# Kernel tuning notes

Hardware: AMD Instinct MI355X
Metric: run time of the kernel (lower is better)

The kernel has to match this reference:

```python
import jax, jax.numpy as jnp
import numpy as np

H = 256
OUT = 2
FANOUT = 10
RES_N = [200000, 50000, 12000, 4096]
USER_N = [250000, 60000, 20000, 8192]
B = RES_N[-1]


def setup_inputs() -> dict:
    key = jax.random.key(0)
    ks = jax.random.split(key, 40)
    ki = iter(ks)
    rng = np.random.default_rng(0)
    inp = {}
    inp["res_x"] = jax.random.normal(next(ki), (RES_N[0], H), jnp.float32)
    inp["user_x"] = jax.random.normal(next(ki), (USER_N[0], H), jnp.float32)
    for name, N in (("res", RES_N), ("user", USER_N)):
        for i in range(3):
            n_src, n_dst = N[i], N[i + 1]
            E = n_dst * FANOUT
            row = jax.random.randint(next(ki), (E,), 0, n_src)   # source node ids
            col = jnp.repeat(jnp.arange(n_dst), FANOUT)          # target node ids
            inp[f"{name}_ei{i}"] = jnp.stack([row, col]).astype(jnp.int32)
    counts = rng.integers(10, 31, size=B)                        # ragged users per restaurant
    T = int(counts.sum())
    inp["num_users_per_res"] = jnp.asarray(counts, jnp.int32)
    inp["inverse_idx"] = jax.random.randint(next(ki), (T,), 0, USER_N[-1])

    def lin(k, fi, fo):
        return jax.random.normal(k, (fo, fi), jnp.float32) / np.sqrt(fi)

    for name in ("res", "user"):
        for i in range(3):
            inp[f"{name}_Wl{i}"] = lin(next(ki), H, H)
            inp[f"{name}_bl{i}"] = jnp.zeros((H,), jnp.float32)
            inp[f"{name}_Wr{i}"] = lin(next(ki), H, H)
    inp["W_out"] = lin(next(ki), 2 * H, OUT)
    inp["b_out"] = jnp.zeros((OUT,), jnp.float32)
    return inp


def sage_conv(x_src, x_tgt, edge_index, Wl, bl, Wr):
    """PyG SAGEConv (aggr='mean', bipartite): lin_l(mean_j x_j) + lin_r(x_tgt)."""
    n_tgt = x_tgt.shape[0]
    msgs = x_src[edge_index[0]]                                            # [E, H] gather
    s = jax.ops.segment_sum(msgs, edge_index[1], num_segments=n_tgt)      # [n_tgt, H]
    cnt = jax.ops.segment_sum(jnp.ones((edge_index.shape[1],), x_src.dtype),
                              edge_index[1], num_segments=n_tgt)
    agg = s / jnp.maximum(cnt, 1.0)[:, None]
    return agg @ Wl.T + bl + x_tgt @ Wr.T


def gnn_forward(x, eis, params, N):
    # ReLU (and dropout, identity in eval) applied when i != num_layers-1 == 1
    for i, (ei, (Wl, bl, Wr)) in enumerate(zip(eis, params)):
        x_tgt = x[: N[i + 1]]
        x = sage_conv(x, x_tgt, ei, Wl, bl, Wr)
        if i != 1:
            x = jax.nn.relu(x)
    return x


def reference(res_x, user_x,
              res_ei0, res_ei1, res_ei2,
              user_ei0, user_ei1, user_ei2,
              inverse_idx, num_users_per_res,
              res_Wl0, res_bl0, res_Wr0,
              res_Wl1, res_bl1, res_Wr1,
              res_Wl2, res_bl2, res_Wr2,
              user_Wl0, user_bl0, user_Wr0,
              user_Wl1, user_bl1, user_Wr1,
              user_Wl2, user_bl2, user_Wr2,
              W_out, b_out):
    res_params = [(res_Wl0, res_bl0, res_Wr0), (res_Wl1, res_bl1, res_Wr1), (res_Wl2, res_bl2, res_Wr2)]
    user_params = [(user_Wl0, user_bl0, user_Wr0), (user_Wl1, user_bl1, user_Wr1), (user_Wl2, user_bl2, user_Wr2)]
    res_out = gnn_forward(res_x, (res_ei0, res_ei1, res_ei2), res_params, RES_N)      # [B, H]
    user_out = gnn_forward(user_x, (user_ei0, user_ei1, user_ei2), user_params, USER_N)  # [M, H]
    # ragged segment-mean pooling: split by num_users_per_res, mean each group
    u = user_out[inverse_idx]                                              # [T, H]
    T = inverse_idx.shape[0]
    seg_ids = jnp.repeat(jnp.arange(B), num_users_per_res, total_repeat_length=T)
    pooled = jax.ops.segment_sum(u, seg_ids, num_segments=B)
    pooled = pooled / num_users_per_res.astype(pooled.dtype)[:, None]      # [B, H]
    emb = jnp.concatenate([res_out, pooled], axis=1)                       # [B, 2H]
    return emb @ W_out.T + b_out
```

## Files before the change

kernel.cpp:

```cpp
#include <hip/hip_runtime.h>

#define H 256
#define FANOUT 10

typedef __attribute__((ext_vector_type(8))) short bf16x8;
typedef __attribute__((ext_vector_type(4))) float f32x4;

__device__ __forceinline__ unsigned short f2bf(float x) {
  unsigned int u = __float_as_uint(x);
  u += 0x7FFFu + ((u >> 16) & 1u);
  return (unsigned short)(u >> 16);
}
__device__ __forceinline__ float bf2f(unsigned short h) {
  return __uint_as_float(((unsigned int)h) << 16);
}

struct PtrPack { const float* p[12]; };

__global__ __launch_bounds__(256) void wprep_kernel(PtrPack pk,
                                                    unsigned short* __restrict__ WB) {
  int g = blockIdx.x * 256 + threadIdx.x;
  int mat = g >> 16;
  int e = g & 65535;
  float x = pk.p[mat][e];
  unsigned short h = f2bf(x);
  float r = x - bf2f(h);
  WB[(size_t)mat * 131072 + e] = h;
  WB[(size_t)mat * 131072 + 65536 + e] = f2bf(r);
}

__global__ __launch_bounds__(256) void agg_kernel(
    const float* __restrict__ src, const int* __restrict__ row,
    float* __restrict__ agg, int n_tgt) {
  const int t = blockIdx.x * 4 + (threadIdx.x >> 6);
  if (t >= n_tgt) return;
  const int lane = threadIdx.x & 63;
  const int base = t * FANOUT;
  float4 acc = {0.f, 0.f, 0.f, 0.f};
#pragma unroll
  for (int k = 0; k < FANOUT; ++k) {
    int r = row[base + k];
    const float4 v =
        *reinterpret_cast<const float4*>(src + (size_t)r * H + lane * 4);
    acc.x += v.x; acc.y += v.y; acc.z += v.z; acc.w += v.w;
  }
  acc.x *= 0.1f; acc.y *= 0.1f; acc.z *= 0.1f; acc.w *= 0.1f;
  *reinterpret_cast<float4*>(agg + (size_t)t * H + lane * 4) = acc;
}

__global__ __launch_bounds__(256, 2) void sage_gemm_mfma(
    const float* __restrict__ Af, const float* __restrict__ Xf,
    const unsigned short* __restrict__ Wl2, const unsigned short* __restrict__ Wr2,
    const float* __restrict__ bias, float* __restrict__ Out,
    int n_tgt, int relu) {
  __shared__ unsigned short lds[2][2][4 * 64 * 8];
  const int tid = threadIdx.x;
  const int lane = tid & 63, wc = tid >> 6;
  const int l15 = lane & 15, lk = lane >> 4;
  const int m0 = blockIdx.x * 64;
  const int srow = tid >> 2, sch = tid & 3;
  const int grow = m0 + srow;
  const bool sok = grow < n_tgt;
  const int ldsoff = (((srow >> 4) * 64) + (srow & 15) + sch * 16) * 8;

  f32x4 acc[4][4];
#pragma unroll
  for (int i = 0; i < 4; ++i)
#pragma unroll
    for (int j = 0; j < 4; ++j) acc[i][j] = (f32x4){0.f, 0.f, 0.f, 0.f};

  float4 f0 = {0, 0, 0, 0}, f1 = {0, 0, 0, 0};
  auto gload = [&](int s) {
    if (sok) {
      const float* S = (s >> 3) ? Xf : Af;
      const float* p = S + (size_t)grow * H + (s & 7) * 32 + sch * 8;
      f0 = *reinterpret_cast<const float4*>(p);
      f1 = *reinterpret_cast<const float4*>(p + 4);
    } else {
      f0 = (float4){0, 0, 0, 0};
      f1 = (float4){0, 0, 0, 0};
    }
  };
  auto sconv = [&](int buf) {
    const float xs[8] = {f0.x, f0.y, f0.z, f0.w, f1.x, f1.y, f1.z, f1.w};
    bf16x8 vh, vl;
#pragma unroll
    for (int i = 0; i < 8; ++i) {
      unsigned short h = f2bf(xs[i]);
      vh[i] = (short)h;
      vl[i] = (short)f2bf(xs[i] - bf2f(h));
    }
    *reinterpret_cast<bf16x8*>(&lds[buf][0][ldsoff]) = vh;
    *reinterpret_cast<bf16x8*>(&lds[buf][1][ldsoff]) = vl;
  };

  gload(0);
  sconv(0);
  __syncthreads();

  for (int s = 0; s < 16; ++s) {
    const int buf = s & 1;
    if (s < 15) gload(s + 1);
    const int kt = (s & 7) * 32;
    const unsigned short* __restrict__ W = (s >> 3) ? Wr2 : Wl2;
    bf16x8 bh[4], bl[4];
#pragma unroll
    for (int nf = 0; nf < 4; ++nf) {
      const int off = (wc * 64 + nf * 16 + l15) * H + kt + lk * 8;
      bh[nf] = *reinterpret_cast<const bf16x8*>(W + off);
      bl[nf] = *reinterpret_cast<const bf16x8*>(W + 65536 + off);
    }
    bf16x8 ah[4], al[4];
#pragma unroll
    for (int mf = 0; mf < 4; ++mf) {
      const int o = (mf * 64 + lane) * 8;
      ah[mf] = *reinterpret_cast<const bf16x8*>(&lds[buf][0][o]);
      al[mf] = *reinterpret_cast<const bf16x8*>(&lds[buf][1][o]);
    }
#pragma unroll
    for (int mf = 0; mf < 4; ++mf)
#pragma unroll
      for (int nf = 0; nf < 4; ++nf) {
        acc[mf][nf] = __builtin_amdgcn_mfma_f32_16x16x32_bf16(ah[mf], bh[nf], acc[mf][nf], 0, 0, 0);
        acc[mf][nf] = __builtin_amdgcn_mfma_f32_16x16x32_bf16(ah[mf], bl[nf], acc[mf][nf], 0, 0, 0);
        acc[mf][nf] = __builtin_amdgcn_mfma_f32_16x16x32_bf16(al[mf], bh[nf], acc[mf][nf], 0, 0, 0);
      }
    if (s < 15) sconv(buf ^ 1);
    __syncthreads();
  }

#pragma unroll
  for (int nf = 0; nf < 4; ++nf) {
    const int c = wc * 64 + nf * 16 + l15;
    const float bv = bias[c];
#pragma unroll
    for (int mf = 0; mf < 4; ++mf) {
      const int r0 = m0 + mf * 16 + lk * 4;
#pragma unroll
      for (int j = 0; j < 4; ++j) {
        const int r = r0 + j;
        if (r < n_tgt) {
          float v = acc[mf][nf][j] + bv;
          if (relu) v = fmaxf(v, 0.f);
          Out[(size_t)r * H + c] = v;
        }
      }
    }
  }
}

__global__ __launch_bounds__(1024) void scan_kernel(
    const int* __restrict__ cnt, int* __restrict__ off, int B) {
  __shared__ int sdata[1024];
  const int t = threadIdx.x;
  const int base = t * 4;
  int c[4];
#pragma unroll
  for (int k = 0; k < 4; ++k) c[k] = (base + k < B) ? cnt[base + k] : 0;
  int s0 = c[0];
  int s1 = s0 + c[1];
  int s2 = s1 + c[2];
  int s3 = s2 + c[3];
  sdata[t] = s3;
  __syncthreads();
  for (int o = 1; o < 1024; o <<= 1) {
    int v = (t >= o) ? sdata[t - o] : 0;
    __syncthreads();
    sdata[t] += v;
    __syncthreads();
  }
  int excl = sdata[t] - s3;
  if (base + 0 < B) off[base + 0] = excl;
  if (base + 1 < B) off[base + 1] = excl + s0;
  if (base + 2 < B) off[base + 2] = excl + s1;
  if (base + 3 < B) off[base + 3] = excl + s2;
  if (t == 1023) off[B] = sdata[1023];
}

__global__ __launch_bounds__(256) void pool_kernel(
    const float* __restrict__ uo, const int* __restrict__ idx,
    const int* __restrict__ off, const int* __restrict__ cnt,
    float* __restrict__ pooled) {
  const int b = blockIdx.x * 4 + (threadIdx.x >> 6);
  const int lane = threadIdx.x & 63;
  const int o = off[b];
  const int n = cnt[b];
  float4 acc = {0.f, 0.f, 0.f, 0.f};
  for (int k = 0; k < n; ++k) {
    int u = idx[o + k];
    const float4 v =
        *reinterpret_cast<const float4*>(uo + (size_t)u * H + lane * 4);
    acc.x += v.x; acc.y += v.y; acc.z += v.z; acc.w += v.w;
  }
  const float inv = 1.0f / (float)n;
  acc.x *= inv; acc.y *= inv; acc.z *= inv; acc.w *= inv;
  *reinterpret_cast<float4*>(pooled + (size_t)b * H + lane * 4) = acc;
}

__global__ __launch_bounds__(256) void out_kernel(
    const float* __restrict__ res_out, const float* __restrict__ pooled,
    const float* __restrict__ Wout, const float* __restrict__ bout,
    float* __restrict__ out) {
  const int b = blockIdx.x;
  const int t = threadIdx.x;
  const float e0 = res_out[(size_t)b * H + t];
  const float e1 = pooled[(size_t)b * H + t];
  float p0 = e0 * Wout[t] + e1 * Wout[256 + t];
  float p1 = e0 * Wout[512 + t] + e1 * Wout[768 + t];
#pragma unroll
  for (int o = 32; o >= 1; o >>= 1) {
    p0 += __shfl_down(p0, o, 64);
    p1 += __shfl_down(p1, o, 64);
  }
  __shared__ float s0[4], s1[4];
  const int w = t >> 6, lane = t & 63;
  if (lane == 0) { s0[w] = p0; s1[w] = p1; }
  __syncthreads();
  if (t == 0) out[(size_t)b * 2 + 0] = s0[0] + s0[1] + s0[2] + s0[3] + bout[0];
  if (t == 1) out[(size_t)b * 2 + 1] = s1[0] + s1[1] + s1[2] + s1[3] + bout[1];
}

extern "C" void kernel_launch(void* const* d_in, const int* in_sizes, int n_in,
                              void* d_out, int out_size, void* d_ws,
                              size_t ws_size, hipStream_t stream) {
  const float* res_x  = (const float*)d_in[0];
  const float* user_x = (const float*)d_in[1];
  const int* res_ei[3]  = {(const int*)d_in[2], (const int*)d_in[3], (const int*)d_in[4]};
  const int* user_ei[3] = {(const int*)d_in[5], (const int*)d_in[6], (const int*)d_in[7]};

  const int* counts;
  const int* inv_idx;
  if (in_sizes[8] == 4096) { counts = (const int*)d_in[8]; inv_idx = (const int*)d_in[9]; }
  else                     { counts = (const int*)d_in[9]; inv_idx = (const int*)d_in[8]; }

  const float* rW[9]; const float* uW[9];
  for (int i = 0; i < 9; ++i) rW[i] = (const float*)d_in[10 + i];
  for (int i = 0; i < 9; ++i) uW[i] = (const float*)d_in[19 + i];
  const float* Wout = (const float*)d_in[28];
  const float* bout = (const float*)d_in[29];

  float* ws = (float*)d_ws;
  float* AGG  = ws;
  float* B1   = AGG  + (size_t)60000 * H;
  float* B2   = B1   + (size_t)60000 * H;
  float* U3   = B2   + (size_t)20000 * H;
  float* R3   = U3   + (size_t)8192  * H;
  float* POOL = R3   + (size_t)4096  * H;
  unsigned short* WB = (unsigned short*)(POOL + (size_t)4096 * H);
  int* OFF = (int*)(WB + (size_t)12 * 131072);

  PtrPack pk;
  pk.p[0] = uW[0]; pk.p[1] = uW[2];
  pk.p[2] = uW[3]; pk.p[3] = uW[5];
  pk.p[4] = uW[6]; pk.p[5] = uW[8];
  pk.p[6] = rW[0]; pk.p[7] = rW[2];
  pk.p[8] = rW[3]; pk.p[9] = rW[5];
  pk.p[10] = rW[6]; pk.p[11] = rW[8];
  wprep_kernel<<<3072, 256, 0, stream>>>(pk, WB);

  auto Wm = [&](int m) { return WB + (size_t)m * 131072; };
  auto gemm_grid = [](int n) { return (n + 63) / 64; };
  auto agg_grid = [](int n) { return (n + 3) / 4; };

  agg_kernel<<<agg_grid(60000), 256, 0, stream>>>(user_x, user_ei[0], AGG, 60000);
  sage_gemm_mfma<<<gemm_grid(60000), 256, 0, stream>>>(
      AGG, user_x, Wm(0), Wm(1), uW[1], B1, 60000, 1);
  agg_kernel<<<agg_grid(20000), 256, 0, stream>>>(B1, user_ei[1], AGG, 20000);
  sage_gemm_mfma<<<gemm_grid(20000), 256, 0, stream>>>(
      AGG, B1, Wm(2), Wm(3), uW[4], B2, 20000, 0);
  agg_kernel<<<agg_grid(8192), 256, 0, stream>>>(B2, user_ei[2], AGG, 8192);
  sage_gemm_mfma<<<gemm_grid(8192), 256, 0, stream>>>(
      AGG, B2, Wm(4), Wm(5), uW[7], U3, 8192, 1);

  agg_kernel<<<agg_grid(50000), 256, 0, stream>>>(res_x, res_ei[0], AGG, 50000);
  sage_gemm_mfma<<<gemm_grid(50000), 256, 0, stream>>>(
      AGG, res_x, Wm(6), Wm(7), rW[1], B1, 50000, 1);
  agg_kernel<<<agg_grid(12000), 256, 0, stream>>>(B1, res_ei[1], AGG, 12000);
  sage_gemm_mfma<<<gemm_grid(12000), 256, 0, stream>>>(
      AGG, B1, Wm(8), Wm(9), rW[4], B2, 12000, 0);
  agg_kernel<<<agg_grid(4096), 256, 0, stream>>>(B2, res_ei[2], AGG, 4096);
  sage_gemm_mfma<<<gemm_grid(4096), 256, 0, stream>>>(
      AGG, B2, Wm(10), Wm(11), rW[7], R3, 4096, 1);

  scan_kernel<<<1, 1024, 0, stream>>>(counts, OFF, 4096);
  pool_kernel<<<1024, 256, 0, stream>>>(U3, inv_idx, OFF, counts, POOL);
  out_kernel<<<4096, 256, 0, stream>>>(R3, POOL, Wout, bout, (float*)d_out);
}
```

Baseline: 1.068 ms.

## Batch user and restaurant GNN layers into joint launches, prefetch weights, fuse pool+out

Each SAGE layer's aggregation and GEMM for the user and restaurant towers now run in a single launch, with the tower chosen per block. This halves the number of launches and fills the GPU better on the small later layers. The GEMM main loop is unrolled by two and double-buffers the bf16 weight fragments in registers, so global weight loads overlap the MFMAs. Pooling and the output projection are fused into one kernel where four waves split each segment, removing the pooled intermediate buffer. The cost is a larger workspace, since per-tower buffers are no longer reused, and higher register pressure in the GEMM.

```diff
diff --git a/kernel.cpp b/kernel.cpp
--- a/kernel.cpp
+++ b/kernel.cpp
@@ -29,11 +29,23 @@
   WB[(size_t)mat * 131072 + 65536 + e] = f2bf(r);
 }
 
-__global__ __launch_bounds__(256) void agg_kernel(
-    const float* __restrict__ src, const int* __restrict__ row,
-    float* __restrict__ agg, int n_tgt) {
-  const int t = blockIdx.x * 4 + (threadIdx.x >> 6);
-  if (t >= n_tgt) return;
+__global__ __launch_bounds__(256) void agg_pair(
+    const float* __restrict__ srcU, const int* __restrict__ rowU,
+    float* __restrict__ aggU, int nU4,
+    const float* __restrict__ srcR, const int* __restrict__ rowR,
+    float* __restrict__ aggR) {
+  const int blk = blockIdx.x;
+  const float* __restrict__ src;
+  const int* __restrict__ row;
+  float* __restrict__ agg;
+  int t;
+  if (blk < nU4) {
+    src = srcU; row = rowU; agg = aggU;
+    t = blk * 4 + (threadIdx.x >> 6);
+  } else {
+    src = srcR; row = rowR; agg = aggR;
+    t = (blk - nU4) * 4 + (threadIdx.x >> 6);
+  }
   const int lane = threadIdx.x & 63;
   const int base = t * FANOUT;
   float4 acc = {0.f, 0.f, 0.f, 0.f};
@@ -49,15 +61,28 @@
 }
 
 __global__ __launch_bounds__(256, 2) void sage_gemm_mfma(
-    const float* __restrict__ Af, const float* __restrict__ Xf,
-    const unsigned short* __restrict__ Wl2, const unsigned short* __restrict__ Wr2,
-    const float* __restrict__ bias, float* __restrict__ Out,
-    int n_tgt, int relu) {
+    const float* __restrict__ AfU, const float* __restrict__ XfU,
+    const unsigned short* __restrict__ WlU, const unsigned short* __restrict__ WrU,
+    const float* __restrict__ bU, float* __restrict__ OutU, int nU,
+    const float* __restrict__ AfR, const float* __restrict__ XfR,
+    const unsigned short* __restrict__ WlR, const unsigned short* __restrict__ WrR,
+    const float* __restrict__ bR, float* __restrict__ OutR, int nR,
+    int relu) {
   __shared__ unsigned short lds[2][2][4 * 64 * 8];
+  const int nbU = (nU + 63) >> 6;
+  const bool isU = (int)blockIdx.x < nbU;
+  const float* __restrict__ Af = isU ? AfU : AfR;
+  const float* __restrict__ Xf = isU ? XfU : XfR;
+  const unsigned short* __restrict__ Wl2 = isU ? WlU : WlR;
+  const unsigned short* __restrict__ Wr2 = isU ? WrU : WrR;
+  const float* __restrict__ bias = isU ? bU : bR;
+  float* __restrict__ Out = isU ? OutU : OutR;
+  const int n_tgt = isU ? nU : nR;
+  const int m0 = (isU ? (int)blockIdx.x : (int)blockIdx.x - nbU) * 64;
+
   const int tid = threadIdx.x;
   const int lane = tid & 63, wc = tid >> 6;
   const int l15 = lane & 15, lk = lane >> 4;
-  const int m0 = blockIdx.x * 64;
   const int srow = tid >> 2, sch = tid & 3;
   const int grow = m0 + srow;
   const bool sok = grow < n_tgt;
@@ -93,30 +118,25 @@
     *reinterpret_cast<bf16x8*>(&lds[buf][0][ldsoff]) = vh;
     *reinterpret_cast<bf16x8*>(&lds[buf][1][ldsoff]) = vl;
   };
-
-  gload(0);
-  sconv(0);
-  __syncthreads();
-
-  for (int s = 0; s < 16; ++s) {
-    const int buf = s & 1;
-    if (s < 15) gload(s + 1);
+  auto loadB = [&](int s, bf16x8* bh, bf16x8* bl) {
+    const unsigned short* __restrict__ W = (s >> 3) ? Wr2 : Wl2;
     const int kt = (s & 7) * 32;
-    const unsigned short* __restrict__ W = (s >> 3) ? Wr2 : Wl2;
-    bf16x8 bh[4], bl[4];
 #pragma unroll
     for (int nf = 0; nf < 4; ++nf) {
       const int off = (wc * 64 + nf * 16 + l15) * H + kt + lk * 8;
       bh[nf] = *reinterpret_cast<const bf16x8*>(W + off);
       bl[nf] = *reinterpret_cast<const bf16x8*>(W + 65536 + off);
     }
-    bf16x8 ah[4], al[4];
+  };
+  auto dsreadA = [&](int buf, bf16x8* ah, bf16x8* al) {
 #pragma unroll
     for (int mf = 0; mf < 4; ++mf) {
       const int o = (mf * 64 + lane) * 8;
       ah[mf] = *reinterpret_cast<const bf16x8*>(&lds[buf][0][o]);
       al[mf] = *reinterpret_cast<const bf16x8*>(&lds[buf][1][o]);
     }
+  };
+  auto mfma16 = [&](bf16x8* ah, bf16x8* al, bf16x8* bh, bf16x8* bl) {
 #pragma unroll
     for (int mf = 0; mf < 4; ++mf)
 #pragma unroll
@@ -125,8 +145,39 @@
         acc[mf][nf] = __builtin_amdgcn_mfma_f32_16x16x32_bf16(ah[mf], bl[nf], acc[mf][nf], 0, 0, 0);
         acc[mf][nf] = __builtin_amdgcn_mfma_f32_16x16x32_bf16(al[mf], bh[nf], acc[mf][nf], 0, 0, 0);
       }
-    if (s < 15) sconv(buf ^ 1);
-    __syncthreads();
+  };
+
+  bf16x8 bh0[4], bl0[4], bh1[4], bl1[4];
+  bf16x8 ah[4], al[4];
+
+  gload(0);
+  sconv(0);
+  loadB(0, bh0, bl0);
+  __syncthreads();
+
+  for (int ss = 0; ss < 8; ++ss) {
+    {
+      const int s = 2 * ss;
+      gload(s + 1);
+      loadB(s + 1, bh1, bl1);
+      dsreadA(0, ah, al);
+      mfma16(ah, al, bh0, bl0);
+      sconv(1);
+      __syncthreads();
+    }
+    {
+      const int s = 2 * ss + 1;
+      if (s < 15) {
+        gload(s + 1);
+        loadB(s + 1, bh0, bl0);
+      }
+      dsreadA(1, ah, al);
+      mfma16(ah, al, bh1, bl1);
+      if (s < 15) {
+        sconv(0);
+        __syncthreads();
+      }
+    }
   }
 
 #pragma unroll
@@ -177,43 +228,37 @@
   if (t == 1023) off[B] = sdata[1023];
 }
 
-__global__ __launch_bounds__(256) void pool_kernel(
+__global__ __launch_bounds__(256) void poolout_kernel(
     const float* __restrict__ uo, const int* __restrict__ idx,
     const int* __restrict__ off, const int* __restrict__ cnt,
-    float* __restrict__ pooled) {
-  const int b = blockIdx.x * 4 + (threadIdx.x >> 6);
-  const int lane = threadIdx.x & 63;
-  const int o = off[b];
-  const int n = cnt[b];
+    const float* __restrict__ res_out,
+    const float* __restrict__ Wout, const float* __restrict__ bout,
+    float* __restrict__ out) {
+  const int b = blockIdx.x;
+  const int t = threadIdx.x;
+  const int w = t >> 6, lane = t & 63;
+  const int o = off[b], n = cnt[b];
   float4 acc = {0.f, 0.f, 0.f, 0.f};
-  for (int k = 0; k < n; ++k) {
+  for (int k = w; k < n; k += 4) {
     int u = idx[o + k];
     const float4 v =
         *reinterpret_cast<const float4*>(uo + (size_t)u * H + lane * 4);
     acc.x += v.x; acc.y += v.y; acc.z += v.z; acc.w += v.w;
   }
+  __shared__ float pl[4][256];
+  *reinterpret_cast<float4*>(&pl[w][lane * 4]) = acc;
+  __syncthreads();
   const float inv = 1.0f / (float)n;
-  acc.x *= inv; acc.y *= inv; acc.z *= inv; acc.w *= inv;
-  *reinterpret_cast<float4*>(pooled + (size_t)b * H + lane * 4) = acc;
-}
-
-__global__ __launch_bounds__(256) void out_kernel(
-    const float* __restrict__ res_out, const float* __restrict__ pooled,
-    const float* __restrict__ Wout, const float* __restrict__ bout,
-    float* __restrict__ out) {
-  const int b = blockIdx.x;
-  const int t = threadIdx.x;
+  const float e1 = (pl[0][t] + pl[1][t] + pl[2][t] + pl[3][t]) * inv;
   const float e0 = res_out[(size_t)b * H + t];
-  const float e1 = pooled[(size_t)b * H + t];
   float p0 = e0 * Wout[t] + e1 * Wout[256 + t];
   float p1 = e0 * Wout[512 + t] + e1 * Wout[768 + t];
 #pragma unroll
-  for (int o = 32; o >= 1; o >>= 1) {
-    p0 += __shfl_down(p0, o, 64);
-    p1 += __shfl_down(p1, o, 64);
+  for (int od = 32; od >= 1; od >>= 1) {
+    p0 += __shfl_down(p0, od, 64);
+    p1 += __shfl_down(p1, od, 64);
   }
   __shared__ float s0[4], s1[4];
-  const int w = t >> 6, lane = t & 63;
   if (lane == 0) { s0[w] = p0; s1[w] = p1; }
   __syncthreads();
   if (t == 0) out[(size_t)b * 2 + 0] = s0[0] + s0[1] + s0[2] + s0[3] + bout[0];
@@ -240,13 +285,15 @@
   const float* bout = (const float*)d_in[29];
 
   float* ws = (float*)d_ws;
-  float* AGG  = ws;
-  float* B1   = AGG  + (size_t)60000 * H;
-  float* B2   = B1   + (size_t)60000 * H;
-  float* U3   = B2   + (size_t)20000 * H;
+  float* AGGU = ws;
+  float* AGGR = AGGU + (size_t)60000 * H;
+  float* UB1  = AGGR + (size_t)50000 * H;
+  float* RB1  = UB1  + (size_t)60000 * H;
+  float* UB2  = RB1  + (size_t)50000 * H;
+  float* RB2  = UB2  + (size_t)20000 * H;
+  float* U3   = RB2  + (size_t)12000 * H;
   float* R3   = U3   + (size_t)8192  * H;
-  float* POOL = R3   + (size_t)4096  * H;
-  unsigned short* WB = (unsigned short*)(POOL + (size_t)4096 * H);
+  unsigned short* WB = (unsigned short*)(R3 + (size_t)4096 * H);
   int* OFF = (int*)(WB + (size_t)12 * 131072);
 
   PtrPack pk;
@@ -259,30 +306,27 @@
   wprep_kernel<<<3072, 256, 0, stream>>>(pk, WB);
 
   auto Wm = [&](int m) { return WB + (size_t)m * 131072; };
-  auto gemm_grid = [](int n) { return (n + 63) / 64; };
-  auto agg_grid = [](int n) { return (n + 3) / 4; };
-
-  agg_kernel<<<agg_grid(60000), 256, 0, stream>>>(user_x, user_ei[0], AGG, 60000);
-  sage_gemm_mfma<<<gemm_grid(60000), 256, 0, stream>>>(
-      AGG, user_x, Wm(0), Wm(1), uW[1], B1, 60000, 1);
-  agg_kernel<<<agg_grid(20000), 256, 0, stream>>>(B1, user_ei[1], AGG, 20000);
-  sage_gemm_mfma<<<gemm_grid(20000), 256, 0, stream>>>(
-      AGG, B1, Wm(2), Wm(3), uW[4], B2, 20000, 0);
-  agg_kernel<<<agg_grid(8192), 256, 0, stream>>>(B2, user_ei[2], AGG, 8192);
-  sage_gemm_mfma<<<gemm_grid(8192), 256, 0, stream>>>(
-      AGG, B2, Wm(4), Wm(5), uW[7], U3, 8192, 1);
-
-  agg_kernel<<<agg_grid(50000), 256, 0, stream>>>(res_x, res_ei[0], AGG, 50000);
-  sage_gemm_mfma<<<gemm_grid(50000), 256, 0, stream>>>(
-      AGG, res_x, Wm(6), Wm(7), rW[1], B1, 50000, 1);
-  agg_kernel<<<agg_grid(12000), 256, 0, stream>>>(B1, res_ei[1], AGG, 12000);
-  sage_gemm_mfma<<<gemm_grid(12000), 256, 0, stream>>>(
-      AGG, B1, Wm(8), Wm(9), rW[4], B2, 12000, 0);
-  agg_kernel<<<agg_grid(4096), 256, 0, stream>>>(B2, res_ei[2], AGG, 4096);
-  sage_gemm_mfma<<<gemm_grid(4096), 256, 0, stream>>>(
-      AGG, B2, Wm(10), Wm(11), rW[7], R3, 4096, 1);
+  auto gb = [](int n) { return (n + 63) / 64; };
+
+  agg_pair<<<15000 + 12500, 256, 0, stream>>>(user_x, user_ei[0], AGGU, 15000,
+                                              res_x, res_ei[0], AGGR);
+  sage_gemm_mfma<<<gb(60000) + gb(50000), 256, 0, stream>>>(
+      AGGU, user_x, Wm(0), Wm(1), uW[1], UB1, 60000,
+      AGGR, res_x,  Wm(6), Wm(7), rW[1], RB1, 50000, 1);
+
+  agg_pair<<<5000 + 3000, 256, 0, stream>>>(UB1, user_ei[1], AGGU, 5000,
+                                            RB1, res_ei[1], AGGR);
+  sage_gemm_mfma<<<gb(20000) + gb(12000), 256, 0, stream>>>(
+      AGGU, UB1, Wm(2), Wm(3), uW[4], UB2, 20000,
+      AGGR, RB1, Wm(8), Wm(9), rW[4], RB2, 12000, 0);
+
+  agg_pair<<<2048 + 1024, 256, 0, stream>>>(UB2, user_ei[2], AGGU, 2048,
+                                            RB2, res_ei[2], AGGR);
+  sage_gemm_mfma<<<gb(8192) + gb(4096), 256, 0, stream>>>(
+      AGGU, UB2, Wm(4), Wm(5),  uW[7], U3, 8192,
+      AGGR, RB2, Wm(10), Wm(11), rW[7], R3, 4096, 1);
 
   scan_kernel<<<1, 1024, 0, stream>>>(counts, OFF, 4096);
-  pool_kernel<<<1024, 256, 0, stream>>>(U3, inv_idx, OFF, counts, POOL);
-  out_kernel<<<4096, 256, 0, stream>>>(R3, POOL, Wout, bout, (float*)d_out);
-}
+  poolout_kernel<<<4096, 256, 0, stream>>>(U3, inv_idx, OFF, counts, R3,
+                                           Wout, bout, (float*)d_out);
+}
```

After: 942.0 us. 1.13x faster.
